# Optimization experiments

Hardware: AMD Instinct MI355X
Metric: run time of the kernel (lower is better)

Reference implementation:

```python
import jax, jax.numpy as jnp
import numpy as np

B, T, D = 32, 400, 64
EPS = 1e-6


def setup_inputs() -> dict:
    key = jax.random.key(0)
    k1, k2, k3 = jax.random.split(key, 3)
    x = jax.random.normal(k1, (B, T, D), dtype=jnp.float32)
    mu = jax.random.normal(k2, (B, T, D), dtype=jnp.float32)
    # Build SPD covariance matrices: A A^T / D + I
    A = jax.random.normal(k3, (B, T, D, D), dtype=jnp.float32)
    sigma = jnp.einsum('btij,btkj->btik', A, A) / D + jnp.eye(D, dtype=jnp.float32)
    return {"x": x, "mu": mu, "sigma": sigma}


def reference(x, mu, sigma):
    d = sigma.shape[-1]
    # Regularize and factorize: sigma + eps*I = L L^T
    L = jnp.linalg.cholesky(sigma + EPS * jnp.eye(d, dtype=sigma.dtype))  # [B,T,D,D]
    diff = x - mu  # [B,T,D]
    # Solve L z = diff (batched lower-triangular solve)
    z = jax.scipy.linalg.solve_triangular(L, diff[..., None], lower=True)[..., 0]  # [B,T,D]
    log_det = jnp.sum(jnp.log(jnp.diagonal(L, axis1=-2, axis2=-1)), axis=-1)  # [B,T]
    log_prob = -0.5 * jnp.sum(z * z, axis=-1) - log_det - 0.5 * d * jnp.log(2.0 * jnp.pi)
    ll = jnp.mean(jnp.sum(log_prob, axis=1), axis=0)  # sum over time, mean over batch
    return jnp.expand_dims(-ll, axis=-1)  # shape [1]
```

## Files before the change

kernel.cpp:

```cpp
#include <hip/hip_runtime.h>

#define D_   64
#define CH   16
#define NBT_ 12800
#define B_   32

__device__ __forceinline__ float rl(float v, int l) {
    return __uint_as_float(__builtin_amdgcn_readlane(__float_as_uint(v), l));
}

__global__ __launch_bounds__(256) void chol_ll(const float* __restrict__ x,
                                               const float* __restrict__ mu,
                                               const float* __restrict__ sigma,
                                               float* __restrict__ partial) {
    __shared__ float lds[4][3][CH][D_];
    const int lane = threadIdx.x & 63;
    const int wv   = threadIdx.x >> 6;
    const int bt   = blockIdx.x * 4 + wv;

    const float* base = sigma + (size_t)bt * (D_ * D_) + (size_t)lane * D_;
    float d = x[bt * D_ + lane] - mu[bt * D_ + lane];
    float q = 0.f, lg = 0.f;

    #pragma unroll
    for (int t = 0; t < 4; ++t) {
        float cur[CH];
        const float4* p = (const float4*)(base + t * CH);
        #pragma unroll
        for (int r = 0; r < 4; ++r) {
            float4 v = p[r];
            cur[4 * r + 0] = v.x; cur[4 * r + 1] = v.y;
            cur[4 * r + 2] = v.z; cur[4 * r + 3] = v.w;
        }
        #pragma unroll
        for (int m = 0; m < t; ++m) {
            float tmp[CH];
            #pragma unroll
            for (int k = 0; k < CH; ++k) tmp[k] = lds[wv][m][k][lane];
            #pragma unroll
            for (int k = 0; k < CH; ++k) {
                #pragma unroll
                for (int c = 0; c < CH; ++c)
                    cur[c] = __builtin_fmaf(-tmp[k], rl(tmp[k], t * CH + c), cur[c]);
            }
        }
        #pragma unroll
        for (int kk = 0; kk < CH; ++kk) {
            const int gk = t * CH + kk;
            float s   = rl(cur[kk], gk) + 1e-6f;
            float inv = __builtin_amdgcn_rsqf(s);
            lg += __builtin_amdgcn_logf(s);
            cur[kk] *= inv;
            float zk = rl(d, gk) * inv;
            q += zk * zk;
            d = __builtin_fmaf(-cur[kk], zk, d);
            #pragma unroll
            for (int c = kk + 1; c < CH; ++c)
                cur[c] = __builtin_fmaf(-cur[kk], rl(cur[kk], t * CH + c), cur[c]);
        }
        if (t < 3) {
            #pragma unroll
            for (int c = 0; c < CH; ++c) lds[wv][t][c][lane] = cur[c];
        }
    }

    if (lane == 0) {
        float log_det = 0.34657359027997264f * lg;
        float lp = -0.5f * q - log_det - 58.81206612509905f;
        partial[bt] = lp;
    }
}

__global__ __launch_bounds__(1024) void reduce_ll(const float* __restrict__ partial,
                                                  float* __restrict__ out) {
    float s = 0.f;
    for (int i = threadIdx.x; i < NBT_; i += 1024) s += partial[i];
    #pragma unroll
    for (int off = 32; off > 0; off >>= 1) s += __shfl_down(s, off, 64);
    __shared__ float ws[16];
    const int lane = threadIdx.x & 63, w = threadIdx.x >> 6;
    if (lane == 0) ws[w] = s;
    __syncthreads();
    if (threadIdx.x == 0) {
        float t = 0.f;
        #pragma unroll
        for (int i = 0; i < 16; ++i) t += ws[i];
        out[0] = -t / (float)B_;
    }
}

extern "C" void kernel_launch(void* const* d_in, const int* in_sizes, int n_in,
                              void* d_out, int out_size, void* d_ws, size_t ws_size,
                              hipStream_t stream) {
    const float* x     = (const float*)d_in[0];
    const float* mu    = (const float*)d_in[1];
    const float* sigma = (const float*)d_in[2];
    float* partial = (float*)d_ws;
    chol_ll<<<NBT_ / 4, 256, 0, stream>>>(x, mu, sigma, partial);
    reduce_ll<<<1, 1024, 0, stream>>>(partial, (float*)d_out);
}
```

Baseline: 357.9 us.

## Use two 32-column panels for per-wave Cholesky instead of four 16-column panels

Switches the blocked right-looking Cholesky from four 16-column panels to two 32-column panels. Only one LDS panel is stored and the trailing update reads it back one column at a time, with the next LDS load prefetched. This cuts LDS traffic and the number of panel passes, and shrinks LDS use. The cost is roughly twice as many live registers for the current panel, which may reduce occupancy.

```diff
diff --git a/kernel.cpp b/kernel.cpp
--- a/kernel.cpp
+++ b/kernel.cpp
@@ -1,7 +1,7 @@
 #include <hip/hip_runtime.h>
 
 #define D_   64
-#define CH   16
+#define CH   32
 #define NBT_ 12800
 #define B_   32
 
@@ -13,7 +13,7 @@
                                                const float* __restrict__ mu,
                                                const float* __restrict__ sigma,
                                                float* __restrict__ partial) {
-    __shared__ float lds[4][3][CH][D_];
+    __shared__ float lds[4][CH][D_];
     const int lane = threadIdx.x & 63;
     const int wv   = threadIdx.x >> 6;
     const int bt   = blockIdx.x * 4 + wv;
@@ -22,31 +22,53 @@
     float d = x[bt * D_ + lane] - mu[bt * D_ + lane];
     float q = 0.f, lg = 0.f;
 
-    #pragma unroll
-    for (int t = 0; t < 4; ++t) {
-        float cur[CH];
-        const float4* p = (const float4*)(base + t * CH);
+    float cur[CH];
+
+    {
+        const float4* p = (const float4*)base;
         #pragma unroll
-        for (int r = 0; r < 4; ++r) {
+        for (int r = 0; r < CH / 4; ++r) {
             float4 v = p[r];
             cur[4 * r + 0] = v.x; cur[4 * r + 1] = v.y;
             cur[4 * r + 2] = v.z; cur[4 * r + 3] = v.w;
         }
         #pragma unroll
-        for (int m = 0; m < t; ++m) {
-            float tmp[CH];
+        for (int kk = 0; kk < CH; ++kk) {
+            float s   = rl(cur[kk], kk) + 1e-6f;
+            float inv = __builtin_amdgcn_rsqf(s);
+            lg += __builtin_amdgcn_logf(s);
+            cur[kk] *= inv;
+            float zk = rl(d, kk) * inv;
+            q += zk * zk;
+            d = __builtin_fmaf(-cur[kk], zk, d);
             #pragma unroll
-            for (int k = 0; k < CH; ++k) tmp[k] = lds[wv][m][k][lane];
+            for (int c = kk + 1; c < CH; ++c)
+                cur[c] = __builtin_fmaf(-cur[kk], rl(cur[kk], c), cur[c]);
+        }
+        #pragma unroll
+        for (int k = 0; k < CH; ++k) lds[wv][k][lane] = cur[k];
+    }
+
+    {
+        const float4* p = (const float4*)(base + CH);
+        #pragma unroll
+        for (int r = 0; r < CH / 4; ++r) {
+            float4 v = p[r];
+            cur[4 * r + 0] = v.x; cur[4 * r + 1] = v.y;
+            cur[4 * r + 2] = v.z; cur[4 * r + 3] = v.w;
+        }
+        float tn = lds[wv][0][lane];
+        #pragma unroll
+        for (int k = 0; k < CH; ++k) {
+            float tk = tn;
+            if (k + 1 < CH) tn = lds[wv][k + 1][lane];
             #pragma unroll
-            for (int k = 0; k < CH; ++k) {
-                #pragma unroll
-                for (int c = 0; c < CH; ++c)
-                    cur[c] = __builtin_fmaf(-tmp[k], rl(tmp[k], t * CH + c), cur[c]);
-            }
+            for (int c = 0; c < CH; ++c)
+                cur[c] = __builtin_fmaf(-tk, rl(tk, CH + c), cur[c]);
         }
         #pragma unroll
         for (int kk = 0; kk < CH; ++kk) {
-            const int gk = t * CH + kk;
+            const int gk = CH + kk;
             float s   = rl(cur[kk], gk) + 1e-6f;
             float inv = __builtin_amdgcn_rsqf(s);
             lg += __builtin_amdgcn_logf(s);
@@ -56,11 +78,7 @@
             d = __builtin_fmaf(-cur[kk], zk, d);
             #pragma unroll
             for (int c = kk + 1; c < CH; ++c)
-                cur[c] = __builtin_fmaf(-cur[kk], rl(cur[kk], t * CH + c), cur[c]);
-        }
-        if (t < 3) {
-            #pragma unroll
-            for (int c = 0; c < CH; ++c) lds[wv][t][c][lane] = cur[c];
+                cur[c] = __builtin_fmaf(-cur[kk], rl(cur[kk], CH + c), cur[c]);
         }
     }
 
```

Result: no change. 362.1 us (+1.2%).
